# Performance work log

Hardware: AMD Instinct MI355X
Metric: run time of the kernel (lower is better)

## Reference

```python
import jax, jax.numpy as jnp
import numpy as np
from math import sqrt

B, NQ, SK, ISIZE, HSIZE, OSIZE, H = 4, 2048, 2048, 1024, 1024, 1024, 16
D = HSIZE // H  # attn_dim = 64
IEPS = 1e-32
NEG = -1e32

def setup_inputs() -> dict:
    key = jax.random.key(0)
    ks = jax.random.split(key, 9)
    scale = 1.0 / sqrt(ISIZE)
    return {
        "iQ": jax.random.normal(ks[0], (B, NQ, ISIZE), jnp.float32),
        "iK": jax.random.normal(ks[1], (B, SK, ISIZE), jnp.float32),
        "iV": jax.random.normal(ks[2], (B, SK, ISIZE), jnp.float32),
        "mask": jax.random.randint(ks[3], (B, NQ, SK), 0, 2).astype(bool),
        # torch nn.Linear weights: [out_features, in_features]
        "Wq": jax.random.normal(ks[4], (HSIZE, ISIZE), jnp.float32) * scale,
        "Wk": jax.random.normal(ks[5], (HSIZE, ISIZE), jnp.float32) * scale,
        "Wv": jax.random.normal(ks[6], (HSIZE, ISIZE), jnp.float32) * scale,
        "Wo": jax.random.normal(ks[7], (OSIZE, HSIZE), jnp.float32) * scale,
        "sn_bias": jnp.zeros((1,), jnp.float32),  # SparseNormer bias
    }

def reference(iQ, iK, iV, mask, Wq, Wk, Wv, Wo, sn_bias):
    b, nq, _ = iQ.shape
    sk = iK.shape[1]
    # projections, split into heads: [b, h, n, d]
    q = (iQ @ Wq.T).reshape(b, nq, H, D).transpose(0, 2, 1, 3)
    k = (iK @ Wk.T).reshape(b, sk, H, D).transpose(0, 2, 1, 3)
    v = (iV @ Wv.T).reshape(b, sk, H, D).transpose(0, 2, 1, 3)
    # scaled dot-product scores: [b, h, nq, sk]
    scores = jnp.einsum("bhqd,bhkd->bhqk", q, k) / sqrt(D)
    scores = jnp.where(mask[:, None, :, :], NEG, scores)
    # SparseNormer: relu(x + bias)^2 normalized along last dim
    t = jax.nn.relu(scores + sn_bias)
    t = t * t
    attn = t / (t.sum(-1, keepdims=True) + IEPS)
    o = jnp.einsum("bhqk,bhkd->bhqd", attn, v)
    o = o.transpose(0, 2, 1, 3).reshape(b, nq, HSIZE)
    return o @ Wo.T
```

## Files before the change

### kernel.cpp

```cpp
#include <hip/hip_runtime.h>
#include <stdint.h>

#define B_   4
#define NQ_  2048
#define SK_  2048
#define H_   16
#define HS_  1024
#define D_   64
#define TOKc ((size_t)B_ * NQ_ * HS_)
#define WEc  ((size_t)HS_ * HS_)

typedef __attribute__((ext_vector_type(8))) short bf16x8;
typedef __attribute__((ext_vector_type(4))) float f32x4;
typedef __attribute__((ext_vector_type(2))) float f32x2;
typedef __attribute__((ext_vector_type(8))) unsigned short u16x8;
typedef __attribute__((ext_vector_type(4))) int i32x4;

#define DEVI __device__ __forceinline__

DEVI unsigned short f2bf_hu(float f) {
  union { float f; unsigned int i; } x; x.f = f;
  return (unsigned short)((x.i + 0x8000u) >> 16);
}
DEVI unsigned int pack2(float a, float b) {
  union { float f; unsigned int i; } x, y; x.f = a; y.f = b;
  return __builtin_amdgcn_perm(y.i + 0x8000u, x.i + 0x8000u, 0x07060302u);
}
DEVI u16x8 cvt8(f32x4 lo, f32x4 hi) {
  union { u16x8 s; unsigned int w[4]; } r;
  r.w[0] = pack2(lo[0], lo[1]);
  r.w[1] = pack2(lo[2], lo[3]);
  r.w[2] = pack2(hi[0], hi[1]);
  r.w[3] = pack2(hi[2], hi[3]);
  return r.s;
}
DEVI void async16(void* lds, const void* g) {
  __builtin_amdgcn_global_load_lds(
      (const __attribute__((address_space(1))) unsigned int*)g,
      (__attribute__((address_space(3))) unsigned int*)lds, 16, 0, 0);
}

DEVI f32x2 pkfma(f32x2 a, f32x2 b, f32x2 c) {
  f32x2 d;
  asm("v_pk_fma_f32 %0, %1, %2, %3" : "=v"(d) : "v"(a), "v"(b), "v"(c));
  return d;
}
DEVI f32x2 pkmul(f32x2 a, f32x2 b) {
  f32x2 d;
  asm("v_pk_mul_f32 %0, %1, %2" : "=v"(d) : "v"(a), "v"(b));
  return d;
}
DEVI f32x2 pkadd(f32x2 a, f32x2 b) {
  f32x2 d;
  asm("v_pk_add_f32 %0, %1, %2" : "=v"(d) : "v"(a), "v"(b));
  return d;
}
DEVI unsigned int cvtpk_bf16(float lo, float hi) {
  unsigned int r;
  asm("v_cvt_pk_bf16_f32 %0, %1, %2" : "=v"(r) : "v"(lo), "v"(hi));
  return r;
}
template <int OFF>
DEVI float keepf(float x, unsigned int nb) {
  int k;
  asm("v_bfe_i32 %0, %1, %2, 1" : "=v"(k) : "v"(nb), "i"(OFF));
  union { float f; int i; } u; u.f = x; u.i &= k;
  return u.f;
}

#define SWZB(row, colb) ((((row) * 128) + (colb)) ^ (((row) & 7) << 4))

__global__ __launch_bounds__(256)
void cvt_prep(const float* __restrict__ a, unsigned short* __restrict__ ab,
              const float* __restrict__ wsrc, unsigned short* __restrict__ wdst,
              int naBlocks) {
  const int bi = blockIdx.x;
  const float* s; unsigned short* d; size_t base;
  if (bi < naBlocks) { s = a;    d = ab;   base = (size_t)bi * 2048; }
  else               { s = wsrc; d = wdst; base = (size_t)(bi - naBlocks) * 2048; }
  const size_t o = base + (size_t)threadIdx.x * 8;
  f32x4 lo = *(const f32x4*)(s + o);
  f32x4 hi = *(const f32x4*)(s + o + 4);
  *(u16x8*)(d + o) = cvt8(lo, hi);
}

__global__ __launch_bounds__(256)
void cvt_all(const float* __restrict__ iQ, const float* __restrict__ iK,
             const float* __restrict__ iV, const float* __restrict__ Wq,
             const float* __restrict__ Wk, const float* __restrict__ Wv,
             const float* __restrict__ Wo, unsigned short* __restrict__ ACT,
             unsigned short* __restrict__ WALL) {
  const int bi = blockIdx.x;
  const float* s; unsigned short* d; size_t base;
  if (bi < 12288) {
    const int which = bi >> 12;
    s = (which == 0) ? iQ : (which == 1) ? iK : iV;
    d = ACT + (size_t)which * TOKc;
    base = (size_t)(bi & 4095) * 2048;
  } else {
    const int wi = (bi - 12288) >> 9;
    s = (wi == 0) ? Wq : (wi == 1) ? Wk : (wi == 2) ? Wv : Wo;
    d = WALL + (size_t)wi * WEc;
    base = (size_t)((bi - 12288) & 511) * 2048;
  }
  const size_t o = base + (size_t)threadIdx.x * 8;
  f32x4 lo = *(const f32x4*)(s + o);
  f32x4 hi = *(const f32x4*)(s + o + 4);
  *(u16x8*)(d + o) = cvt8(lo, hi);
}

__global__ __launch_bounds__(256)
void pack_mask(const int* __restrict__ m, unsigned long long* __restrict__ bits) {
  const size_t tid = (size_t)blockIdx.x * 256 + threadIdx.x;
  const unsigned long long bal = __ballot(m[tid] != 0);
  if ((threadIdx.x & 63) == 0) bits[tid >> 6] = bal;
}

template <bool CF32>
DEVI void gemm8_body(const unsigned short* __restrict__ A,
                     const unsigned short* __restrict__ W,
                     void* __restrict__ Cp, int M, int N, int K, char* Lds) {
  const int t = threadIdx.x;
  const int w = t >> 6, l = t & 63;
  const int lm = l & 15, lg = l >> 4;
  const int bm = blockIdx.x * 256, bn = blockIdx.y * 256;
  const int wm = (w >> 2) * 128;
  const int wn = (w & 3) * 64;

  const int sr8 = l >> 3;
  const int scol = ((l & 7) ^ sr8) * 8;
  const unsigned short* gA00 = A + (size_t)(bm +       w * 16 +     sr8) * K + scol;
  const unsigned short* gA01 = A + (size_t)(bm +       w * 16 + 8 + sr8) * K + scol;
  const unsigned short* gA10 = A + (size_t)(bm + 128 + w * 16 +     sr8) * K + scol;
  const unsigned short* gA11 = A + (size_t)(bm + 128 + w * 16 + 8 + sr8) * K + scol;
  const unsigned short* gB00 = W + (size_t)(bn +       w * 16 +     sr8) * K + scol;
  const unsigned short* gB01 = W + (size_t)(bn +       w * 16 + 8 + sr8) * K + scol;
  const unsigned short* gB10 = W + (size_t)(bn + 128 + w * 16 +     sr8) * K + scol;
  const unsigned short* gB11 = W + (size_t)(bn + 128 + w * 16 + 8 + sr8) * K + scol;
  const int ldst = w * 2048 + l * 16;

  auto stage2 = [&](int buf, int half, const unsigned short* g0,
                    const unsigned short* g1, int kofs) {
    char* p = Lds + buf * 65536 + half * 16384 + ldst;
    async16(p,        g0 + kofs);
    async16(p + 1024, g1 + kofs);
  };

  auto rdA = [&](int buf, int row, int ks) -> bf16x8 {
    const char* p = Lds + buf * 65536 + (row >> 7) * 16384 + (row & 127) * 128 +
                    ((ks * 64 + lg * 16) ^ ((row & 7) << 4));
    return *(const bf16x8*)p;
  };
  auto rdB = [&](int buf, int row, int ks) -> bf16x8 {
    const char* p = Lds + 32768 + buf * 65536 + (row >> 7) * 16384 +
                    (row & 127) * 128 + ((ks * 64 + lg * 16) ^ ((row & 7) << 4));
    return *(const bf16x8*)p;
  };

  f32x4 acc[8][4] = {};
  const int NT = K >> 6;

  stage2(0, 0, gA00, gA01, 0);
  stage2(0, 2, gB00, gB01, 0);
  stage2(0, 3, gB10, gB11, 0);
  stage2(0, 1, gA10, gA11, 0);
  if (NT > 1) {
    stage2(1, 0, gA00, gA01, 64);
    stage2(1, 2, gB00, gB01, 64);
    asm volatile("s_waitcnt vmcnt(4)" ::: "memory");
  } else {
    asm volatile("s_waitcnt vmcnt(0)" ::: "memory");
  }
  __builtin_amdgcn_sched_barrier(0);
  __builtin_amdgcn_s_barrier();

  for (int tt = 0; tt < NT; tt++) {
    const int cur = tt & 1, nxt = cur ^ 1;
    const bool p1 = (tt + 1 < NT), p2 = (tt + 2 < NT);
    const int ko1 = (tt + 1) * 64, ko2 = (tt + 2) * 64;
    bf16x8 aF[4][2], bF0[2][2], bF1[2][2];

#pragma unroll
    for (int mf = 0; mf < 4; mf++)
#pragma unroll
      for (int ks = 0; ks < 2; ks++)
        aF[mf][ks] = rdA(cur, wm + mf * 16 + lm, ks);
#pragma unroll
    for (int nf = 0; nf < 2; nf++)
#pragma unroll
      for (int ks = 0; ks < 2; ks++)
        bF0[nf][ks] = rdB(cur, wn + nf * 16 + lm, ks);
    if (p1) { stage2(nxt, 3, gB10, gB11, ko1); stage2(nxt, 1, gA10, gA11, ko1); }
    __builtin_amdgcn_s_barrier();
    asm volatile("s_waitcnt lgkmcnt(0)" ::: "memory");
    __builtin_amdgcn_sched_barrier(0);
    __builtin_amdgcn_s_setprio(1);
#pragma unroll
    for (int ks = 0; ks < 2; ks++)
#pragma unroll
      for (int mf = 0; mf < 4; mf++)
#pragma unroll
        for (int nf = 0; nf < 2; nf++)
          acc[mf][nf] = __builtin_amdgcn_mfma_f32_16x16x32_bf16(
              aF[mf][ks], bF0[nf][ks], acc[mf][nf], 0, 0, 0);
    __builtin_amdgcn_s_setprio(0);
    __builtin_amdgcn_s_barrier();

#pragma unroll
    for (int nf = 0; nf < 2; nf++)
#pragma unroll
      for (int ks = 0; ks < 2; ks++)
        bF1[nf][ks] = rdB(cur, wn + (nf + 2) * 16 + lm, ks);
    __builtin_amdgcn_s_barrier();
    asm volatile("s_waitcnt lgkmcnt(0)" ::: "memory");
    __builtin_amdgcn_sched_barrier(0);
    __builtin_amdgcn_s_setprio(1);
#pragma unroll
    for (int ks = 0; ks < 2; ks++)
#pragma unroll
      for (int mf = 0; mf < 4; mf++)
#pragma unroll
        for (int nf = 0; nf < 2; nf++)
          acc[mf][nf + 2] = __builtin_amdgcn_mfma_f32_16x16x32_bf16(
              aF[mf][ks], bF1[nf][ks], acc[mf][nf + 2], 0, 0, 0);
    __builtin_amdgcn_s_setprio(0);
    __builtin_amdgcn_s_barrier();

#pragma unroll
    for (int mf = 0; mf < 4; mf++)
#pragma unroll
      for (int ks = 0; ks < 2; ks++)
        aF[mf][ks] = rdA(cur, wm + (mf + 4) * 16 + lm, ks);
    __builtin_amdgcn_s_barrier();
    asm volatile("s_waitcnt lgkmcnt(0)" ::: "memory");
    __builtin_amdgcn_sched_barrier(0);
    __builtin_amdgcn_s_setprio(1);
#pragma unroll
    for (int ks = 0; ks < 2; ks++)
#pragma unroll
      for (int mf = 0; mf < 4; mf++)
#pragma unroll
        for (int nf = 0; nf < 2; nf++)
          acc[mf + 4][nf + 2] = __builtin_amdgcn_mfma_f32_16x16x32_bf16(
              aF[mf][ks], bF1[nf][ks], acc[mf + 4][nf + 2], 0, 0, 0);
    __builtin_amdgcn_s_setprio(0);
    __builtin_amdgcn_s_barrier();
    __builtin_amdgcn_sched_barrier(0);

    if (p2) { stage2(cur, 0, gA00, gA01, ko2); stage2(cur, 2, gB00, gB01, ko2); }
    __builtin_amdgcn_s_setprio(1);
#pragma unroll
    for (int ks = 0; ks < 2; ks++)
#pragma unroll
      for (int mf = 0; mf < 4; mf++)
#pragma unroll
        for (int nf = 0; nf < 2; nf++)
          acc[mf + 4][nf] = __builtin_amdgcn_mfma_f32_16x16x32_bf16(
              aF[mf][ks], bF0[nf][ks], acc[mf + 4][nf], 0, 0, 0);
    __builtin_amdgcn_s_setprio(0);

    if (p2)      { asm volatile("s_waitcnt vmcnt(4)" ::: "memory"); }
    else if (p1) { asm volatile("s_waitcnt vmcnt(0)" ::: "memory"); }
    __builtin_amdgcn_sched_barrier(0);
    __builtin_amdgcn_s_barrier();
  }

#pragma unroll
  for (int mf = 0; mf < 8; mf++)
#pragma unroll
    for (int nf = 0; nf < 4; nf++) {
      const int row = bm + wm + mf * 16 + lg * 4;
      const int col = bn + wn + nf * 16 + lm;
#pragma unroll
      for (int r = 0; r < 4; r++) {
        if constexpr (CF32) {
          ((float*)Cp)[(size_t)(row + r) * N + col] = acc[mf][nf][r];
        } else {
          ((unsigned short*)Cp)[(size_t)(row + r) * N + col] = f2bf_hu(acc[mf][nf][r]);
        }
      }
    }
}

template <bool CF32>
__global__ __launch_bounds__(512)
void gemm8(const unsigned short* __restrict__ A, const unsigned short* __restrict__ W,
           void* __restrict__ Cp, int M, int N, int K) {
  __shared__ __align__(16) char Lds[131072];
  gemm8_body<CF32>(A, W, Cp, M, N, K, Lds);
}

__global__ __launch_bounds__(512)
void gemm8_qkv(const unsigned short* __restrict__ ACT,
               const unsigned short* __restrict__ WALL,
               unsigned short* __restrict__ Qb, unsigned short* __restrict__ Kb,
               unsigned short* __restrict__ Vb, int M, int N, int K) {
  __shared__ __align__(16) char Lds[131072];
  const int z = blockIdx.z;
  const unsigned short* A = ACT + (size_t)z * (size_t)M * (size_t)K;
  const unsigned short* W = WALL + (size_t)z * (size_t)N * (size_t)K;
  unsigned short* C = (z == 0) ? Qb : ((z == 1) ? Kb : Vb);
  gemm8_body<false>(A, W, (void*)C, M, N, K, Lds);
}

template <bool CF32>
DEVI void gemm_body_pipe(const unsigned short* __restrict__ A,
                         const unsigned short* __restrict__ Wb,
                         void* __restrict__ Cp, int M, int N, int K,
                         unsigned short* As, unsigned short* Bs) {
  const int t = threadIdx.x;
  const int w = t >> 6, l = t & 63;
  const int lm = l & 15, lg = l >> 4;
  const int bm = blockIdx.x * 128, bn = blockIdx.y * 128;
  const int wm = (w >> 1) * 64, wn = (w & 1) * 64;

  const int sr = t >> 2;
  const int sg = ((t & 3) ^ ((t >> 3) & 3)) * 8;
  const unsigned short* Ag0 = A + (size_t)(bm + sr) * K + sg;
  const unsigned short* Ag1 = A + (size_t)(bm + sr + 64) * K + sg;
  const unsigned short* Wg0 = Wb + (size_t)(bn + sr) * K + sg;
  const unsigned short* Wg1 = Wb + (size_t)(bn + sr + 64) * K + sg;

  const int fx = (lm >> 1) & 3;
  f32x4 acc[4][4] = {};

  auto stage = [&](int bi, int k0) {
    unsigned short* la = As + bi * 4096 + t * 8;
    unsigned short* lb = Bs + bi * 4096 + t * 8;
    async16(la,        Ag0 + k0);
    async16(la + 2048, Ag1 + k0);
    async16(lb,        Wg0 + k0);
    async16(lb + 2048, Wg1 + k0);
  };

  stage(0, 0);
  int cur = 0;
  for (int k0 = 0; k0 < K; k0 += 32) {
    if (k0 + 32 < K) {
      stage(cur ^ 1, k0 + 32);
      asm volatile("s_waitcnt vmcnt(4)" ::: "memory");
    } else {
      asm volatile("s_waitcnt vmcnt(0)" ::: "memory");
    }
    __builtin_amdgcn_sched_barrier(0);
    __builtin_amdgcn_s_barrier();
    const unsigned short* Ab = As + cur * 4096;
    const unsigned short* Bb = Bs + cur * 4096;
    bf16x8 aF[4], bF[4];
#pragma unroll
    for (int i = 0; i < 4; i++)
      aF[i] = *(const bf16x8*)&Ab[(wm + i * 16 + lm) * 32 + ((lg ^ fx) * 8)];
#pragma unroll
    for (int i = 0; i < 4; i++)
      bF[i] = *(const bf16x8*)&Bb[(wn + i * 16 + lm) * 32 + ((lg ^ fx) * 8)];
    __builtin_amdgcn_s_setprio(1);
#pragma unroll
    for (int i = 0; i < 4; i++)
#pragma unroll
      for (int j = 0; j < 4; j++)
        acc[i][j] = __builtin_amdgcn_mfma_f32_16x16x32_bf16(aF[i], bF[j], acc[i][j], 0, 0, 0);
    __builtin_amdgcn_s_setprio(0);
    __builtin_amdgcn_s_barrier();
    cur ^= 1;
  }
#pragma unroll
  for (int i = 0; i < 4; i++)
#pragma unroll
    for (int j = 0; j < 4; j++) {
      const int row = bm + wm + i * 16 + lg * 4;
      const int col = bn + wn + j * 16 + lm;
#pragma unroll
      for (int r = 0; r < 4; r++) {
        if constexpr (CF32) {
          ((float*)Cp)[(size_t)(row + r) * N + col] = acc[i][j][r];
        } else {
          ((unsigned short*)Cp)[(size_t)(row + r) * N + col] = f2bf_hu(acc[i][j][r]);
        }
      }
    }
}

template <bool CF32>
__global__ __launch_bounds__(256)
void gemm_bb(const unsigned short* __restrict__ A, const unsigned short* __restrict__ Wb,
             void* __restrict__ Cp, int M, int N, int K) {
  __shared__ unsigned short As[2 * 128 * 32];
  __shared__ unsigned short Bs[2 * 128 * 32];
  gemm_body_pipe<CF32>(A, Wb, Cp, M, N, K, As, Bs);
}

template <bool ABF16, bool CF32>
__global__ __launch_bounds__(256)
void gemm_bt(const void* __restrict__ Ap, const float* __restrict__ W,
             void* __restrict__ Cp, int M, int N, int K) {
  __shared__ unsigned short As[128 * 40];
  __shared__ unsigned short Bs[128 * 40];
  const int t = threadIdx.x;
  const int w = t >> 6, l = t & 63;
  const int lm = l & 15, lg = l >> 4;
  const int bm = blockIdx.x * 128, bn = blockIdx.y * 128;
  const int wm = (w >> 1) * 64, wn = (w & 1) * 64;
  const int sr = t >> 2, sc = (t & 3) * 8;
  const float* Af = (const float*)Ap;
  const unsigned short* Ab = (const unsigned short*)Ap;
  const size_t ao0 = (size_t)(bm + sr) * K + sc;
  const size_t ao1 = (size_t)(bm + sr + 64) * K + sc;
  const size_t wo0 = (size_t)(bn + sr) * K + sc;
  const size_t wo1 = (size_t)(bn + sr + 64) * K + sc;
  auto loadA = [&](size_t off) -> u16x8 {
    if constexpr (ABF16) {
      return *(const u16x8*)(Ab + off);
    } else {
      f32x4 lo = *(const f32x4*)(Af + off);
      f32x4 hi = *(const f32x4*)(Af + off + 4);
      return cvt8(lo, hi);
    }
  };
  auto loadW = [&](size_t off) -> u16x8 {
    f32x4 lo = *(const f32x4*)(W + off);
    f32x4 hi = *(const f32x4*)(W + off + 4);
    return cvt8(lo, hi);
  };
  u16x8 pa0 = loadA(ao0), pa1 = loadA(ao1);
  u16x8 pb0 = loadW(wo0), pb1 = loadW(wo1);
  f32x4 acc[4][4] = {};
  for (int k0 = 0; k0 < K; k0 += 32) {
    *(u16x8*)&As[sr * 40 + sc]        = pa0;
    *(u16x8*)&As[(sr + 64) * 40 + sc] = pa1;
    *(u16x8*)&Bs[sr * 40 + sc]        = pb0;
    *(u16x8*)&Bs[(sr + 64) * 40 + sc] = pb1;
    __syncthreads();
    if (k0 + 32 < K) {
      pa0 = loadA(ao0 + k0 + 32);
      pa1 = loadA(ao1 + k0 + 32);
      pb0 = loadW(wo0 + k0 + 32);
      pb1 = loadW(wo1 + k0 + 32);
    }
    bf16x8 aF[4], bF[4];
#pragma unroll
    for (int i = 0; i < 4; i++)
      aF[i] = *(const bf16x8*)&As[(wm + i * 16 + lm) * 40 + lg * 8];
#pragma unroll
    for (int i = 0; i < 4; i++)
      bF[i] = *(const bf16x8*)&Bs[(wn + i * 16 + lm) * 40 + lg * 8];
#pragma unroll
    for (int i = 0; i < 4; i++)
#pragma unroll
      for (int j = 0; j < 4; j++)
        acc[i][j] = __builtin_amdgcn_mfma_f32_16x16x32_bf16(aF[i], bF[j], acc[i][j], 0, 0, 0);
    __syncthreads();
  }
#pragma unroll
  for (int i = 0; i < 4; i++)
#pragma unroll
    for (int j = 0; j < 4; j++) {
      const int row = bm + wm + i * 16 + lg * 4;
      const int col = bn + wn + j * 16 + lm;
#pragma unroll
      for (int r = 0; r < 4; r++) {
        if constexpr (CF32) {
          ((float*)Cp)[(size_t)(row + r) * N + col] = acc[i][j][r];
        } else {
          ((unsigned short*)Cp)[(size_t)(row + r) * N + col] = f2bf_hu(acc[i][j][r]);
        }
      }
    }
}

template <int MODE>
__global__ __launch_bounds__(256)
void attn_sn(const unsigned short* __restrict__ Qb,
             const unsigned short* __restrict__ Kb,
             const unsigned short* __restrict__ Vb,
             const int* __restrict__ mask,
             const unsigned int* __restrict__ bits,
             const float* __restrict__ snb,
             unsigned short* __restrict__ Ob) {
  __shared__ unsigned short Ks[64 * 64];
  __shared__ unsigned short Vt[64 * 64];
  __shared__ unsigned short Pq[128 * 64];

  const int h = blockIdx.x, qt = blockIdx.y, b = blockIdx.z;
  const int t = threadIdx.x, w = t >> 6, l = t & 63;
  const int lm = l & 15, lg = l >> 4;
  const int q0 = qt * 128;
  const int wk = (w >> 1) * 32;
  const int wn = (w & 1) * 64;
  const float bias = snb[0];

  char* KsB = (char*)Ks;
  char* VtB = (char*)Vt;
  char* PqB = (char*)Pq;

  bf16x8 bQ[4][2];
#pragma unroll
  for (int ni = 0; ni < 4; ni++)
#pragma unroll
    for (int kf = 0; kf < 2; kf++) {
      const int qq = q0 + wn + ni * 16 + lm;
      bQ[ni][kf] = *(const bf16x8*)&Qb[(size_t)(b * NQ_ + qq) * HS_ + h * D_ + kf * 32 + lg * 8];
    }

  const int kr = t >> 3, kcb = (t & 7) * 16;
  const unsigned short* Kg = Kb + (size_t)(b * SK_) * HS_ + h * D_ + (t & 7) * 8;
  const int va = t & 31;
  const int vc = (t >> 5) * 8;
  const unsigned short* Vg = Vb + (size_t)(b * SK_) * HS_ + h * D_ + vc;
  const int* mbase = mask + (size_t)b * NQ_ * SK_;

  f32x4 oacc[2][4] = {};
  float dpart[4] = {0.f, 0.f, 0.f, 0.f};
  f32x2 dp2[4] = {};

  u16x8 pk0 = *(const u16x8*)(Kg + (size_t)(kr) * HS_);
  u16x8 pk1 = *(const u16x8*)(Kg + (size_t)(32 + kr) * HS_);
  u16x8 pv0 = *(const u16x8*)(Vg + (size_t)(2 * va) * HS_);
  u16x8 pv1 = *(const u16x8*)(Vg + (size_t)(2 * va + 1) * HS_);

  for (int kt = 0; kt < SK_ / 64; kt++) {
    const int kk0 = kt * 64;
    *(u16x8*)(KsB + SWZB(kr, kcb))      = pk0;
    *(u16x8*)(KsB + SWZB(kr + 32, kcb)) = pk1;
    {
      union { u16x8 s; unsigned int w4[4]; } a0, a1;
      a0.s = pv0; a1.s = pv1;
#pragma unroll
      for (int ww = 0; ww < 4; ww++) {
        unsigned int lo = __builtin_amdgcn_perm(a1.w4[ww], a0.w4[ww], 0x05040100u);
        unsigned int hi = __builtin_amdgcn_perm(a1.w4[ww], a0.w4[ww], 0x07060302u);
        *(unsigned int*)(VtB + SWZB(vc + 2 * ww,     4 * va)) = lo;
        *(unsigned int*)(VtB + SWZB(vc + 2 * ww + 1, 4 * va)) = hi;
      }
    }
    __syncthreads();

    if (kt + 1 < SK_ / 64) {
      const int nk0 = kk0 + 64;
      pk0 = *(const u16x8*)(Kg + (size_t)(nk0 + kr) * HS_);
      pk1 = *(const u16x8*)(Kg + (size_t)(nk0 + 32 + kr) * HS_);
      pv0 = *(const u16x8*)(Vg + (size_t)(nk0 + 2 * va) * HS_);
      pv1 = *(const u16x8*)(Vg + (size_t)(nk0 + 2 * va + 1) * HS_);
    }

    i32x4 mq[4][2];
    unsigned int mb[4];
    if constexpr (MODE == 1) {
#pragma unroll
      for (int ni = 0; ni < 4; ni++)
        mb[ni] = bits[(size_t)(b * NQ_ + q0 + wn + ni * 16 + lm) * 64 + kt * 2 + (wk >> 5)];
    } else {
#pragma unroll
      for (int ni = 0; ni < 4; ni++) {
        const int* mrow = mbase + (size_t)(q0 + wn + ni * 16 + lm) * SK_ + kk0 + wk + lg * 4;
#pragma unroll
        for (int mi = 0; mi < 2; mi++) mq[ni][mi] = *(const i32x4*)(mrow + mi * 16);
      }
    }

    bf16x8 aK[2][2];
#pragma unroll
    for (int mi = 0; mi < 2; mi++)
#pragma unroll
      for (int kf = 0; kf < 2; kf++)
        aK[mi][kf] = *(const bf16x8*)(KsB + SWZB(wk + mi * 16 + lm, kf * 64 + lg * 16));
    f32x4 sf[2][4] = {};
    __builtin_amdgcn_s_setprio(1);
#pragma unroll
    for (int mi = 0; mi < 2; mi++)
#pragma unroll
      for (int ni = 0; ni < 4; ni++) {
        sf[mi][ni] = __builtin_amdgcn_mfma_f32_16x16x32_bf16(aK[mi][0], bQ[ni][0], sf[mi][ni], 0, 0, 0);
        sf[mi][ni] = __builtin_amdgcn_mfma_f32_16x16x32_bf16(aK[mi][1], bQ[ni][1], sf[mi][ni], 0, 0, 0);
      }
    __builtin_amdgcn_s_setprio(0);

    if constexpr (MODE == 1) {
      const f32x2 c8 = {0.125f, 0.125f};
      const f32x2 bias2 = {bias, bias};
#pragma unroll
      for (int ni = 0; ni < 4; ni++) {
        const unsigned int nb = (~mb[ni]) >> (lg * 4);
#pragma unroll
        for (int mi = 0; mi < 2; mi++) {
          const f32x4 sv = sf[mi][ni];
          f32x2 t01 = pkfma((f32x2){sv[0], sv[1]}, c8, bias2);
          f32x2 t23 = pkfma((f32x2){sv[2], sv[3]}, c8, bias2);
          float x0 = fmaxf(t01[0], 0.f), x1 = fmaxf(t01[1], 0.f);
          float x2 = fmaxf(t23[0], 0.f), x3 = fmaxf(t23[1], 0.f);
          if (mi == 0) {
            x0 = keepf<0>(x0, nb);  x1 = keepf<1>(x1, nb);
            x2 = keepf<2>(x2, nb);  x3 = keepf<3>(x3, nb);
          } else {
            x0 = keepf<16>(x0, nb); x1 = keepf<17>(x1, nb);
            x2 = keepf<18>(x2, nb); x3 = keepf<19>(x3, nb);
          }
          const f32x2 u01 = pkmul((f32x2){x0, x1}, (f32x2){x0, x1});
          const f32x2 u23 = pkmul((f32x2){x2, x3}, (f32x2){x2, x3});
          dp2[ni] = pkadd(dp2[ni], u01);
          dp2[ni] = pkadd(dp2[ni], u23);
          const unsigned long long pk =
              (unsigned long long)cvtpk_bf16(u01[0], u01[1]) |
              ((unsigned long long)cvtpk_bf16(u23[0], u23[1]) << 32);
          *(unsigned long long*)(PqB + SWZB(wn + ni * 16 + lm, (wk + mi * 16 + lg * 4) * 2)) = pk;
        }
      }
    } else {
#pragma unroll
      for (int ni = 0; ni < 4; ni++) {
        float dsum = 0.f;
#pragma unroll
        for (int mi = 0; mi < 2; mi++) {
          const f32x4 sv = sf[mi][ni];
          float x2[4];
#pragma unroll
          for (int r = 0; r < 4; r++) {
            float x = fmaxf(sv[r] * 0.125f + bias, 0.f);
            x = mq[ni][mi][r] ? 0.f : x;
            x2[r] = x * x;
            dsum += x2[r];
          }
          const unsigned long long pk =
              (unsigned long long)pack2(x2[0], x2[1]) |
              ((unsigned long long)pack2(x2[2], x2[3]) << 32);
          *(unsigned long long*)(PqB + SWZB(wn + ni * 16 + lm, (wk + mi * 16 + lg * 4) * 2)) = pk;
        }
        dpart[ni] += dsum;
      }
    }
    __syncthreads();

#pragma unroll
    for (int k2 = 0; k2 < 2; k2++) {
      bf16x8 aV[2], bP[4];
#pragma unroll
      for (int mi = 0; mi < 2; mi++)
        aV[mi] = *(const bf16x8*)(VtB + SWZB(wk + mi * 16 + lm, k2 * 64 + lg * 16));
#pragma unroll
      for (int ni = 0; ni < 4; ni++)
        bP[ni] = *(const bf16x8*)(PqB + SWZB(wn + ni * 16 + lm, k2 * 64 + lg * 16));
      __builtin_amdgcn_s_setprio(1);
#pragma unroll
      for (int mi = 0; mi < 2; mi++)
#pragma unroll
        for (int ni = 0; ni < 4; ni++)
          oacc[mi][ni] = __builtin_amdgcn_mfma_f32_16x16x32_bf16(aV[mi], bP[ni], oacc[mi][ni], 0, 0, 0);
      __builtin_amdgcn_s_setprio(0);
    }
    __syncthreads();
  }

  float* denomS = (float*)Ks;
#pragma unroll
  for (int ni = 0; ni < 4; ni++) {
    float v = (MODE == 1) ? (dp2[ni][0] + dp2[ni][1]) : dpart[ni];
    v += __shfl_xor(v, 16, 64);
    v += __shfl_xor(v, 32, 64);
    dpart[ni] = v;
  }
  if (((w >> 1) == 0) && (lg == 0)) {
#pragma unroll
    for (int ni = 0; ni < 4; ni++) denomS[wn + ni * 16 + lm] = dpart[ni];
  }
  __syncthreads();
  if (((w >> 1) == 1) && (lg == 0)) {
#pragma unroll
    for (int ni = 0; ni < 4; ni++) denomS[wn + ni * 16 + lm] += dpart[ni];
  }
  __syncthreads();

#pragma unroll
  for (int ni = 0; ni < 4; ni++) {
    const int ql = wn + ni * 16 + lm;
    const float inv = 1.0f / (denomS[ql] + 1e-32f);
#pragma unroll
    for (int mi = 0; mi < 2; mi++) {
      const int d0 = wk + mi * 16 + lg * 4;
      const f32x4 ov = oacc[mi][ni];
      const unsigned long long pk =
          (unsigned long long)cvtpk_bf16(ov[0] * inv, ov[1] * inv) |
          ((unsigned long long)cvtpk_bf16(ov[2] * inv, ov[3] * inv) << 32);
      *(unsigned long long*)(PqB + SWZB(ql, d0 * 2)) = pk;
    }
  }
  __syncthreads();
  const int qf = t >> 1;
  unsigned short* orow = Ob + (size_t)(b * NQ_ + q0 + qf) * HS_ + h * D_ + (t & 1) * 32;
#pragma unroll
  for (int j = 0; j < 4; j++) {
    u16x8 vv = *(const u16x8*)(PqB + SWZB(qf, (t & 1) * 64 + j * 16));
    *(u16x8*)(orow + j * 8) = vv;
  }
}

extern "C" void kernel_launch(void* const* d_in, const int* in_sizes, int n_in,
                              void* d_out, int out_size, void* d_ws, size_t ws_size,
                              hipStream_t stream) {
  (void)in_sizes; (void)n_in; (void)out_size;
  const float* iQ  = (const float*)d_in[0];
  const float* iK  = (const float*)d_in[1];
  const float* iV  = (const float*)d_in[2];
  const int*   msk = (const int*)d_in[3];
  const float* Wq  = (const float*)d_in[4];
  const float* Wk  = (const float*)d_in[5];
  const float* Wv  = (const float*)d_in[6];
  const float* Wo  = (const float*)d_in[7];
  const float* snb = (const float*)d_in[8];
  float* out = (float*)d_out;

  const size_t TOK = TOKc;
  const size_t WE  = WEc;
  const size_t BITS_B = (size_t)B_ * NQ_ * SK_ / 8;
  const size_t NEED1 = (3 * TOK + WE) * 2 + BITS_B;
  const size_t NEEDF = (6 * TOK + 4 * WE) * 2 + BITS_B;

  const dim3 gg(64, 8, 1), bb(256, 1, 1);
  const dim3 ga(H_, NQ_ / 128, B_);
  const dim3 g8(32, 4, 1), g83(32, 4, 3), b512(512, 1, 1);
  const int M = B_ * NQ_, N = HS_, K = HS_;

  if (ws_size >= NEEDF) {
    unsigned short* ACT  = (unsigned short*)d_ws;
    unsigned short* WALL = ACT + 3 * TOK;
    unsigned short* Kb   = WALL + 4 * WE;
    unsigned short* Vb   = Kb + TOK;
    unsigned short* Ob   = Vb + TOK;
    unsigned int*  bits  = (unsigned int*)(Ob + TOK);
    unsigned short* Qb   = (unsigned short*)d_out;
    unsigned short* Wob  = WALL + 3 * WE;

    hipLaunchKernelGGL(cvt_all, dim3(14336), bb, 0, stream,
                       iQ, iK, iV, Wq, Wk, Wv, Wo, ACT, WALL);
    hipLaunchKernelGGL(gemm8_qkv, g83, b512, 0, stream,
                       ACT, WALL, Qb, Kb, Vb, M, N, K);
    hipLaunchKernelGGL(pack_mask, dim3(65536), bb, 0, stream,
                       msk, (unsigned long long*)bits);
    hipLaunchKernelGGL((attn_sn<1>), ga, bb, 0, stream,
                       Qb, Kb, Vb, msk, bits, snb, Ob);
    hipLaunchKernelGGL((gemm8<true>), g8, b512, 0, stream,
                       Ob, Wob, (void*)out, M, N, K);
  } else if (ws_size >= NEED1) {
    unsigned short* Kb = (unsigned short*)d_ws;
    unsigned short* Vb = Kb + TOK;
    unsigned short* Ob = Vb + TOK;
    unsigned short* Wb = Ob + TOK;
    unsigned int* bits = (unsigned int*)(Wb + WE);
    unsigned short* out_us = (unsigned short*)d_out;
    unsigned short* Qb  = out_us;
    unsigned short* INb = out_us + TOK;

    hipLaunchKernelGGL(cvt_prep, dim3(4608), bb, 0, stream, iQ, INb, Wq, Wb, 4096);
    hipLaunchKernelGGL((gemm_bb<false>), gg, bb, 0, stream, INb, Wb, (void*)Qb, M, N, K);
    hipLaunchKernelGGL(cvt_prep, dim3(4608), bb, 0, stream, iK, INb, Wk, Wb, 4096);
    hipLaunchKernelGGL((gemm_bb<false>), gg, bb, 0, stream, INb, Wb, (void*)Kb, M, N, K);
    hipLaunchKernelGGL(cvt_prep, dim3(4608), bb, 0, stream, iV, INb, Wv, Wb, 4096);
    hipLaunchKernelGGL((gemm_bb<false>), gg, bb, 0, stream, INb, Wb, (void*)Vb, M, N, K);
    hipLaunchKernelGGL(cvt_prep, dim3(512), bb, 0, stream,
                       (const float*)nullptr, (unsigned short*)nullptr, Wo, Wb, 0);
    hipLaunchKernelGGL(pack_mask, dim3(65536), bb, 0, stream,
                       msk, (unsigned long long*)bits);
    hipLaunchKernelGGL((attn_sn<1>), ga, bb, 0, stream,
                       Qb, Kb, Vb, msk, bits, snb, Ob);
    hipLaunchKernelGGL((gemm_bb<true>), gg, bb, 0, stream, Ob, Wb, (void*)out, M, N, K);
  } else {
    unsigned short *Qb, *Kb, *Vb, *Ob;
    if (ws_size >= 4 * TOK * sizeof(unsigned short)) {
      Qb = (unsigned short*)d_ws;
      Kb = Qb + TOK;
      Vb = Qb + 2 * TOK;
      Ob = Qb + 3 * TOK;
    } else {
      Qb = (unsigned short*)d_out;
      Kb = (unsigned short*)d_ws;
      Vb = Kb + TOK;
      Ob = Kb + 2 * TOK;
    }
    hipLaunchKernelGGL((gemm_bt<false, false>), gg, bb, 0, stream, (const void*)iQ, Wq, (void*)Qb, M, N, K);
    hipLaunchKernelGGL((gemm_bt<false, false>), gg, bb, 0, stream, (const void*)iK, Wk, (void*)Kb, M, N, K);
    hipLaunchKernelGGL((gemm_bt<false, false>), gg, bb, 0, stream, (const void*)iV, Wv, (void*)Vb, M, N, K);
    hipLaunchKernelGGL((attn_sn<0>), ga, bb, 0, stream,
                       Qb, Kb, Vb, msk, (const unsigned int*)nullptr, snb, Ob);
    hipLaunchKernelGGL((gemm_bt<true, true>), gg, bb, 0, stream, (const void*)Ob, Wo, (void*)out, M, N, K);
  }
}
```

Baseline: 446.9 us.

## Fuse mask packing into conversion, XCD-swizzle GEMM tiles, add pipelined attention kernel

Mask bit-packing now runs as extra blocks of the fp32-to-bf16 conversion kernel, which removes one launch. Both GEMM kernels remap block indices so that neighbouring tiles land on the same XCD, aiming for better L2 reuse. A new attention kernel double-buffers score tiles and prefetches K, V and mask bits one to two tiles ahead, so the QK MFMA for the next tile overlaps the softmax of the current one. The cost is higher register pressure in the attention kernel and a more complex schedule.

```diff
diff --git a/kernel.cpp b/kernel.cpp
--- a/kernel.cpp
+++ b/kernel.cpp
@@ -85,12 +85,19 @@
 }
 
 __global__ __launch_bounds__(256)
-void cvt_all(const float* __restrict__ iQ, const float* __restrict__ iK,
-             const float* __restrict__ iV, const float* __restrict__ Wq,
-             const float* __restrict__ Wk, const float* __restrict__ Wv,
-             const float* __restrict__ Wo, unsigned short* __restrict__ ACT,
-             unsigned short* __restrict__ WALL) {
+void cvt_pack(const float* __restrict__ iQ, const float* __restrict__ iK,
+              const float* __restrict__ iV, const float* __restrict__ Wq,
+              const float* __restrict__ Wk, const float* __restrict__ Wv,
+              const float* __restrict__ Wo, const int* __restrict__ m,
+              unsigned short* __restrict__ ACT, unsigned short* __restrict__ WALL,
+              unsigned long long* __restrict__ bits) {
   const int bi = blockIdx.x;
+  if (bi >= 14336) {
+    const size_t tid = (size_t)(bi - 14336) * 256 + threadIdx.x;
+    const unsigned long long bal = __ballot(m[tid] != 0);
+    if ((threadIdx.x & 63) == 0) bits[tid >> 6] = bal;
+    return;
+  }
   const float* s; unsigned short* d; size_t base;
   if (bi < 12288) {
     const int which = bi >> 12;
@@ -119,11 +126,11 @@
 template <bool CF32>
 DEVI void gemm8_body(const unsigned short* __restrict__ A,
                      const unsigned short* __restrict__ W,
-                     void* __restrict__ Cp, int M, int N, int K, char* Lds) {
+                     void* __restrict__ Cp, int M, int N, int K, char* Lds,
+                     int bm, int bn) {
   const int t = threadIdx.x;
   const int w = t >> 6, l = t & 63;
   const int lm = l & 15, lg = l >> 4;
-  const int bm = blockIdx.x * 256, bn = blockIdx.y * 256;
   const int wm = (w >> 2) * 128;
   const int wn = (w & 3) * 64;
 
@@ -145,7 +152,6 @@
     async16(p,        g0 + kofs);
     async16(p + 1024, g1 + kofs);
   };
-
   auto rdA = [&](int buf, int row, int ks) -> bf16x8 {
     const char* p = Lds + buf * 65536 + (row >> 7) * 16384 + (row & 127) * 128 +
                     ((ks * 64 + lg * 16) ^ ((row & 7) << 4));
@@ -282,12 +288,22 @@
     }
 }
 
+DEVI void xcd_tile(int& bm, int& bn) {
+  const int gx = gridDim.x;
+  const int lin = blockIdx.x + gx * blockIdx.y;
+  const int q = (gx * gridDim.y) >> 3;
+  const int sw = (lin & 7) * q + (lin >> 3);
+  bm = (sw % gx) * 256;
+  bn = (sw / gx) * 256;
+}
+
 template <bool CF32>
 __global__ __launch_bounds__(512)
 void gemm8(const unsigned short* __restrict__ A, const unsigned short* __restrict__ W,
            void* __restrict__ Cp, int M, int N, int K) {
   __shared__ __align__(16) char Lds[131072];
-  gemm8_body<CF32>(A, W, Cp, M, N, K, Lds);
+  int bm, bn; xcd_tile(bm, bn);
+  gemm8_body<CF32>(A, W, Cp, M, N, K, Lds, bm, bn);
 }
 
 __global__ __launch_bounds__(512)
@@ -300,7 +316,8 @@
   const unsigned short* A = ACT + (size_t)z * (size_t)M * (size_t)K;
   const unsigned short* W = WALL + (size_t)z * (size_t)N * (size_t)K;
   unsigned short* C = (z == 0) ? Qb : ((z == 1) ? Kb : Vb);
-  gemm8_body<false>(A, W, (void*)C, M, N, K, Lds);
+  int bm, bn; xcd_tile(bm, bn);
+  gemm8_body<false>(A, W, (void*)C, M, N, K, Lds, bm, bn);
 }
 
 template <bool CF32>
@@ -313,17 +330,14 @@
   const int lm = l & 15, lg = l >> 4;
   const int bm = blockIdx.x * 128, bn = blockIdx.y * 128;
   const int wm = (w >> 1) * 64, wn = (w & 1) * 64;
-
   const int sr = t >> 2;
   const int sg = ((t & 3) ^ ((t >> 3) & 3)) * 8;
   const unsigned short* Ag0 = A + (size_t)(bm + sr) * K + sg;
   const unsigned short* Ag1 = A + (size_t)(bm + sr + 64) * K + sg;
   const unsigned short* Wg0 = Wb + (size_t)(bn + sr) * K + sg;
   const unsigned short* Wg1 = Wb + (size_t)(bn + sr + 64) * K + sg;
-
   const int fx = (lm >> 1) & 3;
   f32x4 acc[4][4] = {};
-
   auto stage = [&](int bi, int k0) {
     unsigned short* la = As + bi * 4096 + t * 8;
     unsigned short* lb = Bs + bi * 4096 + t * 8;
@@ -332,7 +346,6 @@
     async16(lb,        Wg0 + k0);
     async16(lb + 2048, Wg1 + k0);
   };
-
   stage(0, 0);
   int cur = 0;
   for (int k0 = 0; k0 < K; k0 += 32) {
@@ -692,6 +705,216 @@
   }
 }
 
+__global__ __launch_bounds__(256)
+void attn_sn2(const unsigned short* __restrict__ Qb,
+              const unsigned short* __restrict__ Kb,
+              const unsigned short* __restrict__ Vb,
+              const unsigned int* __restrict__ bits,
+              const float* __restrict__ snb,
+              unsigned short* __restrict__ Ob) {
+  __shared__ unsigned short Ks[2][64 * 64];
+  __shared__ unsigned short Vt[64 * 64];
+  __shared__ unsigned short Pq[128 * 64];
+
+  const int h = blockIdx.x, qt = blockIdx.y, b = blockIdx.z;
+  const int t = threadIdx.x, w = t >> 6, l = t & 63;
+  const int lm = l & 15, lg = l >> 4;
+  const int q0 = qt * 128;
+  const int wk = (w >> 1) * 32;
+  const int wn = (w & 1) * 64;
+  const float b8 = snb[0] * 8.0f;
+
+  char* KsB = (char*)Ks;
+  char* VtB = (char*)Vt;
+  char* PqB = (char*)Pq;
+
+  bf16x8 bQ[4][2];
+#pragma unroll
+  for (int ni = 0; ni < 4; ni++)
+#pragma unroll
+    for (int kf = 0; kf < 2; kf++) {
+      const int qq = q0 + wn + ni * 16 + lm;
+      bQ[ni][kf] = *(const bf16x8*)&Qb[(size_t)(b * NQ_ + qq) * HS_ + h * D_ + kf * 32 + lg * 8];
+    }
+
+  const int kr = t >> 3, kcb = (t & 7) * 16;
+  const unsigned short* Kg = Kb + (size_t)(b * SK_) * HS_ + h * D_ + (t & 7) * 8;
+  const int va = t & 31;
+  const int vc = (t >> 5) * 8;
+  const unsigned short* Vg = Vb + (size_t)(b * SK_) * HS_ + h * D_ + vc;
+  const size_t bitbase = (size_t)(b * NQ_ + q0 + wn + lm) * 64 + (wk >> 5);
+
+  f32x4 oacc[2][4] = {};
+  f32x2 dp2[4] = {};
+  f32x4 sfA[2][4], sfB[2][4];
+  unsigned int mbA[4], mbB[4];
+  u16x8 pk0, pk1, pv0, pv1;
+
+  auto qk_tile = [&](int buf, f32x4 (&SN)[2][4]) {
+    bf16x8 aK[2][2];
+#pragma unroll
+    for (int mi = 0; mi < 2; mi++)
+#pragma unroll
+      for (int kf = 0; kf < 2; kf++)
+        aK[mi][kf] = *(const bf16x8*)(KsB + buf * 8192 +
+                                      SWZB(wk + mi * 16 + lm, kf * 64 + lg * 16));
+#pragma unroll
+    for (int mi = 0; mi < 2; mi++)
+#pragma unroll
+      for (int ni = 0; ni < 4; ni++) {
+        SN[mi][ni] = (f32x4){b8, b8, b8, b8};
+        SN[mi][ni] = __builtin_amdgcn_mfma_f32_16x16x32_bf16(aK[mi][0], bQ[ni][0], SN[mi][ni], 0, 0, 0);
+        SN[mi][ni] = __builtin_amdgcn_mfma_f32_16x16x32_bf16(aK[mi][1], bQ[ni][1], SN[mi][ni], 0, 0, 0);
+      }
+  };
+
+  auto softmax = [&](f32x4 (&SC)[2][4], unsigned int (&MC)[4]) {
+#pragma unroll
+    for (int ni = 0; ni < 4; ni++) {
+      const unsigned int nb = (~MC[ni]) >> (lg * 4);
+#pragma unroll
+      for (int mi = 0; mi < 2; mi++) {
+        const f32x4 sv = SC[mi][ni];
+        float x0 = fmaxf(sv[0], 0.f), x1 = fmaxf(sv[1], 0.f);
+        float x2 = fmaxf(sv[2], 0.f), x3 = fmaxf(sv[3], 0.f);
+        if (mi == 0) {
+          x0 = keepf<0>(x0, nb);  x1 = keepf<1>(x1, nb);
+          x2 = keepf<2>(x2, nb);  x3 = keepf<3>(x3, nb);
+        } else {
+          x0 = keepf<16>(x0, nb); x1 = keepf<17>(x1, nb);
+          x2 = keepf<18>(x2, nb); x3 = keepf<19>(x3, nb);
+        }
+        const f32x2 u01 = pkmul((f32x2){x0, x1}, (f32x2){x0, x1});
+        const f32x2 u23 = pkmul((f32x2){x2, x3}, (f32x2){x2, x3});
+        dp2[ni] = pkadd(dp2[ni], u01);
+        dp2[ni] = pkadd(dp2[ni], u23);
+        const unsigned long long pk =
+            (unsigned long long)cvtpk_bf16(u01[0], u01[1]) |
+            ((unsigned long long)cvtpk_bf16(u23[0], u23[1]) << 32);
+        *(unsigned long long*)(PqB + SWZB(wn + ni * 16 + lm, (wk + mi * 16 + lg * 4) * 2)) = pk;
+      }
+    }
+  };
+
+  auto step = [&](int kt, f32x4 (&SC)[2][4], f32x4 (&SN)[2][4],
+                  unsigned int (&MC)[4], unsigned int (&MN)[4]) {
+    const bool more = (kt + 1 < SK_ / 64);
+    const int nxtb = (kt + 1) & 1;
+    if (more) {
+      *(u16x8*)(KsB + nxtb * 8192 + SWZB(kr, kcb))      = pk0;
+      *(u16x8*)(KsB + nxtb * 8192 + SWZB(kr + 32, kcb)) = pk1;
+    }
+    {
+      union { u16x8 s; unsigned int w4[4]; } a0, a1;
+      a0.s = pv0; a1.s = pv1;
+#pragma unroll
+      for (int ww = 0; ww < 4; ww++) {
+        unsigned int lo = __builtin_amdgcn_perm(a1.w4[ww], a0.w4[ww], 0x05040100u);
+        unsigned int hi = __builtin_amdgcn_perm(a1.w4[ww], a0.w4[ww], 0x07060302u);
+        *(unsigned int*)(VtB + SWZB(vc + 2 * ww,     4 * va)) = lo;
+        *(unsigned int*)(VtB + SWZB(vc + 2 * ww + 1, 4 * va)) = hi;
+      }
+    }
+    __syncthreads();
+    if (more) {
+      const int nk = (kt + 1) * 64;
+      pv0 = *(const u16x8*)(Vg + (size_t)(nk + 2 * va) * HS_);
+      pv1 = *(const u16x8*)(Vg + (size_t)(nk + 2 * va + 1) * HS_);
+#pragma unroll
+      for (int ni = 0; ni < 4; ni++)
+        MN[ni] = bits[bitbase + (size_t)ni * 16 * 64 + (kt + 1) * 2];
+    }
+    if (kt + 2 < SK_ / 64) {
+      const int nk2 = (kt + 2) * 64;
+      pk0 = *(const u16x8*)(Kg + (size_t)(nk2 + kr) * HS_);
+      pk1 = *(const u16x8*)(Kg + (size_t)(nk2 + 32 + kr) * HS_);
+    }
+    if (more) qk_tile(nxtb, SN);
+    softmax(SC, MC);
+    __syncthreads();
+#pragma unroll
+    for (int k2 = 0; k2 < 2; k2++) {
+      bf16x8 aV[2], bP[4];
+#pragma unroll
+      for (int mi = 0; mi < 2; mi++)
+        aV[mi] = *(const bf16x8*)(VtB + SWZB(wk + mi * 16 + lm, k2 * 64 + lg * 16));
+#pragma unroll
+      for (int ni = 0; ni < 4; ni++)
+        bP[ni] = *(const bf16x8*)(PqB + SWZB(wn + ni * 16 + lm, k2 * 64 + lg * 16));
+      __builtin_amdgcn_s_setprio(1);
+#pragma unroll
+      for (int mi = 0; mi < 2; mi++)
+#pragma unroll
+        for (int ni = 0; ni < 4; ni++)
+          oacc[mi][ni] = __builtin_amdgcn_mfma_f32_16x16x32_bf16(aV[mi], bP[ni], oacc[mi][ni], 0, 0, 0);
+      __builtin_amdgcn_s_setprio(0);
+    }
+    __syncthreads();
+  };
+
+  pk0 = *(const u16x8*)(Kg + (size_t)(kr) * HS_);
+  pk1 = *(const u16x8*)(Kg + (size_t)(32 + kr) * HS_);
+  *(u16x8*)(KsB + SWZB(kr, kcb))      = pk0;
+  *(u16x8*)(KsB + SWZB(kr + 32, kcb)) = pk1;
+  pv0 = *(const u16x8*)(Vg + (size_t)(2 * va) * HS_);
+  pv1 = *(const u16x8*)(Vg + (size_t)(2 * va + 1) * HS_);
+  __syncthreads();
+  qk_tile(0, sfA);
+  pk0 = *(const u16x8*)(Kg + (size_t)(64 + kr) * HS_);
+  pk1 = *(const u16x8*)(Kg + (size_t)(64 + 32 + kr) * HS_);
+#pragma unroll
+  for (int ni = 0; ni < 4; ni++)
+    mbA[ni] = bits[bitbase + (size_t)ni * 16 * 64];
+
+  for (int kt2 = 0; kt2 < SK_ / 64; kt2 += 2) {
+    step(kt2,     sfA, sfB, mbA, mbB);
+    step(kt2 + 1, sfB, sfA, mbB, mbA);
+  }
+
+  float* denomS = (float*)Ks;
+  float dpart[4];
+#pragma unroll
+  for (int ni = 0; ni < 4; ni++) {
+    float v = dp2[ni][0] + dp2[ni][1];
+    v += __shfl_xor(v, 16, 64);
+    v += __shfl_xor(v, 32, 64);
+    dpart[ni] = v;
+  }
+  if (((w >> 1) == 0) && (lg == 0)) {
+#pragma unroll
+    for (int ni = 0; ni < 4; ni++) denomS[wn + ni * 16 + lm] = dpart[ni];
+  }
+  __syncthreads();
+  if (((w >> 1) == 1) && (lg == 0)) {
+#pragma unroll
+    for (int ni = 0; ni < 4; ni++) denomS[wn + ni * 16 + lm] += dpart[ni];
+  }
+  __syncthreads();
+
+#pragma unroll
+  for (int ni = 0; ni < 4; ni++) {
+    const int ql = wn + ni * 16 + lm;
+    const float inv = 1.0f / (denomS[ql] + 1e-32f);
+#pragma unroll
+    for (int mi = 0; mi < 2; mi++) {
+      const int d0 = wk + mi * 16 + lg * 4;
+      const f32x4 ov = oacc[mi][ni];
+      const unsigned long long pk =
+          (unsigned long long)cvtpk_bf16(ov[0] * inv, ov[1] * inv) |
+          ((unsigned long long)cvtpk_bf16(ov[2] * inv, ov[3] * inv) << 32);
+      *(unsigned long long*)(PqB + SWZB(ql, d0 * 2)) = pk;
+    }
+  }
+  __syncthreads();
+  const int qf = t >> 1;
+  unsigned short* orow = Ob + (size_t)(b * NQ_ + q0 + qf) * HS_ + h * D_ + (t & 1) * 32;
+#pragma unroll
+  for (int j = 0; j < 4; j++) {
+    u16x8 vv = *(const u16x8*)(PqB + SWZB(qf, (t & 1) * 64 + j * 16));
+    *(u16x8*)(orow + j * 8) = vv;
+  }
+}
+
 extern "C" void kernel_launch(void* const* d_in, const int* in_sizes, int n_in,
                               void* d_out, int out_size, void* d_ws, size_t ws_size,
                               hipStream_t stream) {
@@ -728,14 +951,13 @@
     unsigned short* Qb   = (unsigned short*)d_out;
     unsigned short* Wob  = WALL + 3 * WE;
 
-    hipLaunchKernelGGL(cvt_all, dim3(14336), bb, 0, stream,
-                       iQ, iK, iV, Wq, Wk, Wv, Wo, ACT, WALL);
+    hipLaunchKernelGGL(cvt_pack, dim3(79872), bb, 0, stream,
+                       iQ, iK, iV, Wq, Wk, Wv, Wo, msk, ACT, WALL,
+                       (unsigned long long*)bits);
     hipLaunchKernelGGL(gemm8_qkv, g83, b512, 0, stream,
                        ACT, WALL, Qb, Kb, Vb, M, N, K);
-    hipLaunchKernelGGL(pack_mask, dim3(65536), bb, 0, stream,
-                       msk, (unsigned long long*)bits);
-    hipLaunchKernelGGL((attn_sn<1>), ga, bb, 0, stream,
-                       Qb, Kb, Vb, msk, bits, snb, Ob);
+    hipLaunchKernelGGL(attn_sn2, ga, bb, 0, stream,
+                       Qb, Kb, Vb, bits, snb, Ob);
     hipLaunchKernelGGL((gemm8<true>), g8, b512, 0, stream,
                        Ob, Wob, (void*)out, M, N, K);
   } else if (ws_size >= NEED1) {
```

Measured after the change: 516.7 us. +15.6%, slower.
